# Performance work log

Measured on AMD Instinct MI355X. Metric: run time of the kernel, lower is better.

The kernel has to match this reference:

```python
import jax, jax.numpy as jnp
import numpy as np

NX, NY, T, TP, D, C = 1024, 1024, 512, 512, 128, 8


def _make_dtw_path(t_len, p_len, rng):
    """Random monotone warping path matrix from (0,0) to (t_len-1,p_len-1), as in init_DTW_matrix."""
    M = np.zeros((t_len, p_len), dtype=np.float32)
    k, l = 0, 0
    M[0, 0] = 1.0
    while (k < t_len - 1) or (l < p_len - 1):
        if k == t_len - 1:
            l += 1
        elif l == p_len - 1:
            k += 1
        else:
            m = rng.integers(3)
            if m == 0:
                k += 1
            elif m == 1:
                l += 1
            else:
                k += 1
                l += 1
        M[k, l] = 1.0
    return M


def setup_inputs() -> dict:
    key = jax.random.key(0)
    kx, ky, kc = jax.random.split(key, 3)
    X = jax.random.normal(kx, (NX, T, D), dtype=jnp.float32)
    Y = jax.random.normal(ky, (NY, TP, D), dtype=jnp.float32)
    classe = jax.random.randint(kc, (NX,), 0, C, dtype=jnp.int32)
    rng = np.random.default_rng(0)
    pi = jnp.asarray(np.stack([_make_dtw_path(T, TP, rng) for _ in range(C)]))  # [C, T, TP]
    return {"X": X, "Y": Y, "pi": pi, "classe": classe}


def reference(X, Y, pi, classe):
    """Fused OT-DTW l2 cost matrix: mat_cost[i,j] = sum_{t,tp,d} pi[cl(i)][t,tp]*(X[i,t,d]-Y[j,tp,d])^2.
    Equivalent to OTDTW.mat_cost_OT with metric='l2' (multi-dim branch), vectorized over classes."""
    pi_i = pi[classe]                              # [NX, T, TP] per-sample path matrix
    row = pi_i.sum(-1)                             # [NX, T]  row sums of path
    col = pi.sum(1)                                # [C, TP]  column sums per class
    C1 = jnp.einsum('itd,it->i', X * X, row)       # [NX]
    C2 = jnp.einsum('jpd,cp->cj', Y * Y, col)      # [C, NY]
    XP = jnp.einsum('itd,itp->ipd', X, pi_i)       # [NX, TP, D]
    C3 = jnp.einsum('ipd,jpd->ij', XP, Y)          # [NX, NY]
    return C1[:, None] + C2[classe] - 2.0 * C3
```

## Files before the change

kernel.cpp:

```cpp
#include <hip/hip_runtime.h>
#include <hip/hip_bf16.h>
#include <stdint.h>

namespace {

constexpr int kNX = 1024, kNY = 1024, kT = 512, kTP = 512, kD = 128, kC = 8;
constexpr int kK = kTP * kD;
constexpr int SPLITK = 16;
constexpr int KCH = kK / SPLITK;
constexpr int BKT = 64;
constexpr int NT = KCH / BKT;

typedef short bf16x8 __attribute__((ext_vector_type(8)));
typedef float f32x4 __attribute__((ext_vector_type(4)));

constexpr size_t OFF_YB  = 0;
constexpr size_t OFF_XP  = OFF_YB + (size_t)kNY * kK * 2;
constexpr size_t OFF_YS  = OFF_XP + (size_t)kNX * kK * 2;
constexpr size_t OFF_TS  = OFF_YS + (size_t)kNY * kTP * 4;
constexpr size_t OFF_TE  = OFF_TS + (size_t)kC * kTP * 4;
constexpr size_t OFF_C1  = OFF_TE + (size_t)kC * kTP * 4;
constexpr size_t OFF_C2  = OFF_C1 + (size_t)kNX * 4;

__device__ __forceinline__ void gload16(const __hip_bfloat16* g, __hip_bfloat16* l) {
    __builtin_amdgcn_global_load_lds(
        (const __attribute__((address_space(1))) unsigned int*)g,
        (__attribute__((address_space(3))) unsigned int*)l, 16, 0, 0);
}

__device__ __forceinline__ unsigned short bf(float x) {
    union { __hip_bfloat16 h; unsigned short u; } cv;
    cv.h = __float2bfloat16(x);
    return cv.u;
}

__global__ void init_ranges(int* __restrict__ ts, int* __restrict__ te,
                            float* __restrict__ C1) {
    const int idx = blockIdx.x * 256 + threadIdx.x;
    if (idx < kC * kTP) { ts[idx] = 0x7fffffff; te[idx] = -1; }
    if (idx < kNX) C1[idx] = 0.f;
}

__global__ void pi_scan(const float* __restrict__ pi, int* __restrict__ ts,
                        int* __restrict__ te) {
    const int c = blockIdx.y;
    const int tbase = blockIdx.x * 64;
    const int p = threadIdx.x;
    const float* pic = pi + (size_t)c * kT * kTP;
    int tmin = 0x7fffffff, tmax = -1;
    for (int tt = 0; tt < 64; ++tt) {
        const int t = tbase + tt;
        float v = pic[(size_t)t * kTP + p];
        if (v != 0.f) { if (t < tmin) tmin = t; tmax = t; }
    }
    if (tmax >= 0) {
        atomicMin(&ts[c * kTP + p], tmin);
        atomicMax(&te[c * kTP + p], tmax);
    }
}

__global__ void y_prep(const float* __restrict__ Y, __hip_bfloat16* __restrict__ YB,
                       float* __restrict__ YS) {
    const int j = blockIdx.x;
    const int tid = threadIdx.x;
    const int sub = tid & 31, g = tid >> 5;
    const float4* Yj = (const float4*)(Y + (size_t)j * kTP * kD);
    unsigned short* YBj = (unsigned short*)YB + (size_t)j * kTP * kD;
    for (int p = g; p < kTP; p += 8) {
        float4 y = Yj[p * 32 + sub];
        ushort4 o;
        o.x = bf(y.x); o.y = bf(y.y); o.z = bf(y.z); o.w = bf(y.w);
        *(ushort4*)(YBj + p * kD + sub * 4) = o;
        float s = y.x * y.x + y.y * y.y + y.z * y.z + y.w * y.w;
        #pragma unroll
        for (int o2 = 16; o2; o2 >>= 1) s += __shfl_down(s, o2, 32);
        if (sub == 0) YS[(size_t)j * kTP + p] = s;
    }
}

__global__ void c2_kernel(const float* __restrict__ YS, const int* __restrict__ ts,
                          const int* __restrict__ te, float* __restrict__ C2) {
    const int j = blockIdx.x;
    const int lane = threadIdx.x;
    const float* ys = YS + (size_t)j * kTP;
    for (int c = 0; c < kC; ++c) {
        float s = 0.f;
        for (int p = lane; p < kTP; p += 64) {
            float colv = (float)(te[c * kTP + p] - ts[c * kTP + p] + 1);
            s += ys[p] * colv;
        }
        #pragma unroll
        for (int o = 32; o; o >>= 1) s += __shfl_down(s, o);
        if (lane == 0) C2[c * kNY + j] = s;
    }
}

__global__ __launch_bounds__(256) void xp_kernel(const float* __restrict__ X,
                                                 const int* __restrict__ classe,
                                                 const int* __restrict__ ts,
                                                 const int* __restrict__ te,
                                                 float* __restrict__ C1,
                                                 __hip_bfloat16* __restrict__ XPB) {
    const int i = blockIdx.y, pc = blockIdx.x;
    const int tid = threadIdx.x;
    const int sub = tid & 31, g = tid >> 5;
    const int c = classe[i];
    const float4* Xi = (const float4*)(X + (size_t)i * kT * kD);
    unsigned short* XPi = (unsigned short*)XPB + (size_t)i * kTP * kD;
    float sq = 0.f;
    #pragma unroll
    for (int q = 0; q < 8; ++q) {
        const int p = pc * 64 + q * 8 + g;
        const int t0 = ts[c * kTP + p], t1 = te[c * kTP + p];
        float ax = 0.f, ay = 0.f, az = 0.f, aw = 0.f;
        for (int t = t0; t <= t1; ++t) {
            float4 v = Xi[t * 32 + sub];
            ax += v.x; ay += v.y; az += v.z; aw += v.w;
            sq += v.x * v.x + v.y * v.y + v.z * v.z + v.w * v.w;
        }
        ushort4 o;
        o.x = bf(ax); o.y = bf(ay); o.z = bf(az); o.w = bf(aw);
        *(ushort4*)(XPi + p * kD + sub * 4) = o;
    }
    #pragma unroll
    for (int o = 32; o; o >>= 1) sq += __shfl_down(sq, o);
    __shared__ float red[4];
    if ((tid & 63) == 0) red[tid >> 6] = sq;
    __syncthreads();
    if (tid == 0) atomicAdd(&C1[i], red[0] + red[1] + red[2] + red[3]);
}

__global__ void init_out(const float* __restrict__ C1, const float* __restrict__ C2,
                         const int* __restrict__ classe, float* __restrict__ out) {
    const int i = blockIdx.x;
    const float c1 = C1[i];
    const float* c2 = C2 + (size_t)classe[i] * kNY;
    float* o = out + (size_t)i * kNY;
    for (int j = threadIdx.x; j < kNY; j += 256) o[j] = c1 + c2[j];
}

__global__ __launch_bounds__(512, 2) void gemm_c3(const __hip_bfloat16* __restrict__ A,
                                                  const __hip_bfloat16* __restrict__ B,
                                                  float* __restrict__ out) {
    __shared__ __align__(16) char lds[131072];
    __hip_bfloat16* ldsE = (__hip_bfloat16*)lds;

    const int tid = threadIdx.x;
    const int lane = tid & 63, wv = tid >> 6;
    const int wr = wv >> 2, wc = wv & 3;

    const int bid = blockIdx.x;
    const int swz = (bid & 7) * 32 + (bid >> 3);
    const int z = swz >> 4, t16 = swz & 15;
    const int rowBase = (t16 >> 2) * 256;
    const int colBase = (t16 & 3) * 256;
    const size_t k0base = (size_t)z * KCH;

    const int scol = ((tid & 7) * 8) ^ (((tid >> 3) & 7) * 8);
    const __hip_bfloat16* aSrc[4];
    const __hip_bfloat16* bSrc[4];
    int dstE[4];
    #pragma unroll
    for (int q = 0; q < 4; ++q) {
        const int R = q * 64 + (tid >> 3);
        aSrc[q] = A + (size_t)(rowBase + R) * kK + k0base + scol;
        bSrc[q] = B + (size_t)(colBase + R) * kK + k0base + scol;
        dstE[q] = (q * 512 + tid) * 8;
    }

    const int swzR = (lane & 7) << 4;
    const int aLin = (wr * 128 + (lane & 15)) * 128 + ((lane >> 4) << 4);
    const int bLin = (wc * 64 + (lane & 15)) * 128 + ((lane >> 4) << 4);
    const int aB0 = (aLin) ^ swzR, aB1 = (aLin + 64) ^ swzR;
    const int bB0 = (bLin) ^ swzR, bB1 = (bLin + 64) ^ swzR;

    f32x4 acc[8][4] = {};

    #pragma unroll
    for (int q = 0; q < 4; ++q) gload16(aSrc[q], ldsE + dstE[q]);
    #pragma unroll
    for (int q = 0; q < 4; ++q) gload16(bSrc[q], ldsE + 16384 + dstE[q]);

    int buf = 0;
    for (int t = 0; t < NT; ++t) {
        asm volatile("s_waitcnt vmcnt(0)" ::: "memory");
        __builtin_amdgcn_s_barrier();
        asm volatile("" ::: "memory");

        const int koff = (t + 1) * BKT;
        const int bufB = buf * 65536;
        const int nBufE = (buf ^ 1) * 32768;

        if (t + 1 < NT) {
            #pragma unroll
            for (int q = 0; q < 4; ++q) gload16(aSrc[q] + koff, ldsE + nBufE + dstE[q]);
        }

        #pragma unroll
        for (int qd = 0; qd < 4; ++qd) {
            const int mh = qd & 1, nh = qd >> 1;
            bf16x8 af[4][2], bfr[2][2];
            #pragma unroll
            for (int m = 0; m < 4; ++m) {
                af[m][0] = *(const bf16x8*)(lds + bufB + aB0 + mh * 8192 + m * 2048);
                af[m][1] = *(const bf16x8*)(lds + bufB + aB1 + mh * 8192 + m * 2048);
            }
            #pragma unroll
            for (int n = 0; n < 2; ++n) {
                bfr[n][0] = *(const bf16x8*)(lds + bufB + 32768 + bB0 + nh * 4096 + n * 2048);
                bfr[n][1] = *(const bf16x8*)(lds + bufB + 32768 + bB1 + nh * 4096 + n * 2048);
            }
            __builtin_amdgcn_s_setprio(1);
            #pragma unroll
            for (int m = 0; m < 4; ++m)
                #pragma unroll
                for (int n = 0; n < 2; ++n) {
                    acc[mh * 4 + m][nh * 2 + n] = __builtin_amdgcn_mfma_f32_16x16x32_bf16(
                        af[m][0], bfr[n][0], acc[mh * 4 + m][nh * 2 + n], 0, 0, 0);
                    acc[mh * 4 + m][nh * 2 + n] = __builtin_amdgcn_mfma_f32_16x16x32_bf16(
                        af[m][1], bfr[n][1], acc[mh * 4 + m][nh * 2 + n], 0, 0, 0);
                }
            __builtin_amdgcn_s_setprio(0);

            if (qd == 0 && t + 1 < NT) {
                #pragma unroll
                for (int q = 0; q < 4; ++q)
                    gload16(bSrc[q] + koff, ldsE + nBufE + 16384 + dstE[q]);
            }
        }
        buf ^= 1;
    }

    #pragma unroll
    for (int mi = 0; mi < 8; ++mi) {
        #pragma unroll
        for (int ni = 0; ni < 4; ++ni) {
            #pragma unroll
            for (int jj = 0; jj < 4; ++jj) {
                const int R = rowBase + wr * 128 + mi * 16 + (lane >> 4) * 4 + jj;
                const int Cc = colBase + wc * 64 + ni * 16 + (lane & 15);
                atomicAdd(&out[(size_t)R * kNY + Cc], -2.0f * acc[mi][ni][jj]);
            }
        }
    }
}

}

extern "C" void kernel_launch(void* const* d_in, const int* in_sizes, int n_in,
                              void* d_out, int out_size, void* d_ws, size_t ws_size,
                              hipStream_t stream) {
    const float* X = (const float*)d_in[0];
    const float* Y = (const float*)d_in[1];
    const float* pi = (const float*)d_in[2];
    const int* classe = (const int*)d_in[3];
    float* out = (float*)d_out;

    char* ws = (char*)d_ws;
    __hip_bfloat16* YB = (__hip_bfloat16*)(ws + OFF_YB);
    __hip_bfloat16* XPB = (__hip_bfloat16*)(ws + OFF_XP);
    float* YS = (float*)(ws + OFF_YS);
    int* ts = (int*)(ws + OFF_TS);
    int* te = (int*)(ws + OFF_TE);
    float* C1 = (float*)(ws + OFF_C1);
    float* C2 = (float*)(ws + OFF_C2);

    init_ranges<<<(kC * kTP + 255) / 256, 256, 0, stream>>>(ts, te, C1);
    pi_scan<<<dim3(kT / 64, kC), kTP, 0, stream>>>(pi, ts, te);
    y_prep<<<kNY, 256, 0, stream>>>(Y, YB, YS);
    c2_kernel<<<kNY, 64, 0, stream>>>(YS, ts, te, C2);
    xp_kernel<<<dim3(8, kNX), 256, 0, stream>>>(X, classe, ts, te, C1, XPB);
    init_out<<<kNX, 256, 0, stream>>>(C1, C2, classe, out);
    gemm_c3<<<(kNX / 256) * (kNY / 256) * SPLITK, 512, 0, stream>>>(XPB, YB, out);
}
```

Before: 387.6 us.

## Merge Y prep, C2 reduction and XP build into one kernel; fold bias into GEMM

Combines y_prep, c2_kernel and xp_kernel into a single prep_main launch that splits block indices between Y conversion (now computing the C2 per-class sums directly from LDS-cached path counts) and XP accumulation. It drops the YS intermediate buffer. The split-K slice z==0 of the GEMM adds C1+C2 while doing its atomic adds, and a memset replaces init_out. This cuts launches and an extra pass over the output, but adds a per-element bias gather in the GEMM epilogue and a 16KB LDS fill per Y block.

```diff
diff --git a/kernel.cpp b/kernel.cpp
--- a/kernel.cpp
+++ b/kernel.cpp
@@ -16,8 +16,7 @@
 
 constexpr size_t OFF_YB  = 0;
 constexpr size_t OFF_XP  = OFF_YB + (size_t)kNY * kK * 2;
-constexpr size_t OFF_YS  = OFF_XP + (size_t)kNX * kK * 2;
-constexpr size_t OFF_TS  = OFF_YS + (size_t)kNY * kTP * 4;
+constexpr size_t OFF_TS  = OFF_XP + (size_t)kNX * kK * 2;
 constexpr size_t OFF_TE  = OFF_TS + (size_t)kC * kTP * 4;
 constexpr size_t OFF_C1  = OFF_TE + (size_t)kC * kTP * 4;
 constexpr size_t OFF_C2  = OFF_C1 + (size_t)kNX * 4;
@@ -59,88 +58,90 @@
     }
 }
 
-__global__ void y_prep(const float* __restrict__ Y, __hip_bfloat16* __restrict__ YB,
-                       float* __restrict__ YS) {
-    const int j = blockIdx.x;
-    const int tid = threadIdx.x;
-    const int sub = tid & 31, g = tid >> 5;
-    const float4* Yj = (const float4*)(Y + (size_t)j * kTP * kD);
-    unsigned short* YBj = (unsigned short*)YB + (size_t)j * kTP * kD;
-    for (int p = g; p < kTP; p += 8) {
-        float4 y = Yj[p * 32 + sub];
-        ushort4 o;
-        o.x = bf(y.x); o.y = bf(y.y); o.z = bf(y.z); o.w = bf(y.w);
-        *(ushort4*)(YBj + p * kD + sub * 4) = o;
-        float s = y.x * y.x + y.y * y.y + y.z * y.z + y.w * y.w;
-        #pragma unroll
-        for (int o2 = 16; o2; o2 >>= 1) s += __shfl_down(s, o2, 32);
-        if (sub == 0) YS[(size_t)j * kTP + p] = s;
-    }
-}
-
-__global__ void c2_kernel(const float* __restrict__ YS, const int* __restrict__ ts,
-                          const int* __restrict__ te, float* __restrict__ C2) {
-    const int j = blockIdx.x;
-    const int lane = threadIdx.x;
-    const float* ys = YS + (size_t)j * kTP;
-    for (int c = 0; c < kC; ++c) {
-        float s = 0.f;
-        for (int p = lane; p < kTP; p += 64) {
-            float colv = (float)(te[c * kTP + p] - ts[c * kTP + p] + 1);
-            s += ys[p] * colv;
-        }
-        #pragma unroll
-        for (int o = 32; o; o >>= 1) s += __shfl_down(s, o);
-        if (lane == 0) C2[c * kNY + j] = s;
-    }
-}
-
-__global__ __launch_bounds__(256) void xp_kernel(const float* __restrict__ X,
+__global__ __launch_bounds__(256) void prep_main(const float* __restrict__ Y,
+                                                 const float* __restrict__ X,
                                                  const int* __restrict__ classe,
                                                  const int* __restrict__ ts,
                                                  const int* __restrict__ te,
+                                                 __hip_bfloat16* __restrict__ YB,
+                                                 __hip_bfloat16* __restrict__ XPB,
                                                  float* __restrict__ C1,
-                                                 __hip_bfloat16* __restrict__ XPB) {
-    const int i = blockIdx.y, pc = blockIdx.x;
+                                                 float* __restrict__ C2) {
+    const int bid = blockIdx.x;
     const int tid = threadIdx.x;
     const int sub = tid & 31, g = tid >> 5;
-    const int c = classe[i];
-    const float4* Xi = (const float4*)(X + (size_t)i * kT * kD);
-    unsigned short* XPi = (unsigned short*)XPB + (size_t)i * kTP * kD;
-    float sq = 0.f;
-    #pragma unroll
-    for (int q = 0; q < 8; ++q) {
-        const int p = pc * 64 + q * 8 + g;
-        const int t0 = ts[c * kTP + p], t1 = te[c * kTP + p];
-        float ax = 0.f, ay = 0.f, az = 0.f, aw = 0.f;
-        for (int t = t0; t <= t1; ++t) {
-            float4 v = Xi[t * 32 + sub];
-            ax += v.x; ay += v.y; az += v.z; aw += v.w;
-            sq += v.x * v.x + v.y * v.y + v.z * v.z + v.w * v.w;
-        }
-        ushort4 o;
-        o.x = bf(ax); o.y = bf(ay); o.z = bf(az); o.w = bf(aw);
-        *(ushort4*)(XPi + p * kD + sub * 4) = o;
-    }
-    #pragma unroll
-    for (int o = 32; o; o >>= 1) sq += __shfl_down(sq, o);
-    __shared__ float red[4];
-    if ((tid & 63) == 0) red[tid >> 6] = sq;
-    __syncthreads();
-    if (tid == 0) atomicAdd(&C1[i], red[0] + red[1] + red[2] + red[3]);
-}
-
-__global__ void init_out(const float* __restrict__ C1, const float* __restrict__ C2,
-                         const int* __restrict__ classe, float* __restrict__ out) {
-    const int i = blockIdx.x;
-    const float c1 = C1[i];
-    const float* c2 = C2 + (size_t)classe[i] * kNY;
-    float* o = out + (size_t)i * kNY;
-    for (int j = threadIdx.x; j < kNY; j += 256) o[j] = c1 + c2[j];
+
+    if (bid < kNY) {
+        const int j = bid;
+        __shared__ float cntL[kC * kTP];
+        for (int idx = tid; idx < kC * kTP; idx += 256)
+            cntL[idx] = (float)(te[idx] - ts[idx] + 1);
+        __syncthreads();
+
+        const float4* Yj = (const float4*)(Y + (size_t)j * kTP * kD);
+        unsigned short* YBj = (unsigned short*)YB + (size_t)j * kTP * kD;
+        float c2acc[kC] = {};
+        for (int p = g; p < kTP; p += 8) {
+            float4 y = Yj[p * 32 + sub];
+            ushort4 o;
+            o.x = bf(y.x); o.y = bf(y.y); o.z = bf(y.z); o.w = bf(y.w);
+            *(ushort4*)(YBj + p * kD + sub * 4) = o;
+            float s = y.x * y.x + y.y * y.y + y.z * y.z + y.w * y.w;
+            #pragma unroll
+            for (int o2 = 16; o2; o2 >>= 1) s += __shfl_xor(s, o2, 32);
+            if (sub == 0) {
+                #pragma unroll
+                for (int c = 0; c < kC; ++c) c2acc[c] += cntL[c * kTP + p] * s;
+            }
+        }
+        __syncthreads();
+        __shared__ float c2red[8][kC];
+        if (sub == 0) {
+            #pragma unroll
+            for (int c = 0; c < kC; ++c) c2red[g][c] = c2acc[c];
+        }
+        __syncthreads();
+        if (tid < kC) {
+            float s = 0.f;
+            #pragma unroll
+            for (int q = 0; q < 8; ++q) s += c2red[q][tid];
+            C2[tid * kNY + j] = s;
+        }
+    } else {
+        const int b2 = bid - kNY;
+        const int i = b2 >> 3, pc = b2 & 7;
+        const int c = classe[i];
+        const float4* Xi = (const float4*)(X + (size_t)i * kT * kD);
+        unsigned short* XPi = (unsigned short*)XPB + (size_t)i * kTP * kD;
+        float sq = 0.f;
+        #pragma unroll
+        for (int q = 0; q < 8; ++q) {
+            const int p = pc * 64 + q * 8 + g;
+            const int t0 = ts[c * kTP + p], t1 = te[c * kTP + p];
+            float ax = 0.f, ay = 0.f, az = 0.f, aw = 0.f;
+            for (int t = t0; t <= t1; ++t) {
+                float4 v = Xi[t * 32 + sub];
+                ax += v.x; ay += v.y; az += v.z; aw += v.w;
+                sq += v.x * v.x + v.y * v.y + v.z * v.z + v.w * v.w;
+            }
+            ushort4 o;
+            o.x = bf(ax); o.y = bf(ay); o.z = bf(az); o.w = bf(aw);
+            *(ushort4*)(XPi + p * kD + sub * 4) = o;
+        }
+        #pragma unroll
+        for (int o = 32; o; o >>= 1) sq += __shfl_down(sq, o);
+        __shared__ float red[4];
+        if ((tid & 63) == 0) red[tid >> 6] = sq;
+        __syncthreads();
+        if (tid == 0) atomicAdd(&C1[i], red[0] + red[1] + red[2] + red[3]);
+    }
 }
 
 __global__ __launch_bounds__(512, 2) void gemm_c3(const __hip_bfloat16* __restrict__ A,
                                                   const __hip_bfloat16* __restrict__ B,
+                                                  const float* __restrict__ C1,
+                                                  const float* __restrict__ C2,
+                                                  const int* __restrict__ classe,
                                                   float* __restrict__ out) {
     __shared__ __align__(16) char lds[131072];
     __hip_bfloat16* ldsE = (__hip_bfloat16*)lds;
@@ -231,6 +232,7 @@
         buf ^= 1;
     }
 
+    const bool addBase = (z == 0);
     #pragma unroll
     for (int mi = 0; mi < 8; ++mi) {
         #pragma unroll
@@ -239,7 +241,9 @@
             for (int jj = 0; jj < 4; ++jj) {
                 const int R = rowBase + wr * 128 + mi * 16 + (lane >> 4) * 4 + jj;
                 const int Cc = colBase + wc * 64 + ni * 16 + (lane & 15);
-                atomicAdd(&out[(size_t)R * kNY + Cc], -2.0f * acc[mi][ni][jj]);
+                float v = -2.0f * acc[mi][ni][jj];
+                if (addBase) v += C1[R] + C2[(size_t)classe[R] * kNY + Cc];
+                atomicAdd(&out[(size_t)R * kNY + Cc], v);
             }
         }
     }
@@ -259,17 +263,14 @@
     char* ws = (char*)d_ws;
     __hip_bfloat16* YB = (__hip_bfloat16*)(ws + OFF_YB);
     __hip_bfloat16* XPB = (__hip_bfloat16*)(ws + OFF_XP);
-    float* YS = (float*)(ws + OFF_YS);
     int* ts = (int*)(ws + OFF_TS);
     int* te = (int*)(ws + OFF_TE);
     float* C1 = (float*)(ws + OFF_C1);
     float* C2 = (float*)(ws + OFF_C2);
 
+    hipMemsetAsync(out, 0, (size_t)out_size * sizeof(float), stream);
     init_ranges<<<(kC * kTP + 255) / 256, 256, 0, stream>>>(ts, te, C1);
     pi_scan<<<dim3(kT / 64, kC), kTP, 0, stream>>>(pi, ts, te);
-    y_prep<<<kNY, 256, 0, stream>>>(Y, YB, YS);
-    c2_kernel<<<kNY, 64, 0, stream>>>(YS, ts, te, C2);
-    xp_kernel<<<dim3(8, kNX), 256, 0, stream>>>(X, classe, ts, te, C1, XPB);
-    init_out<<<kNX, 256, 0, stream>>>(C1, C2, classe, out);
-    gemm_c3<<<(kNX / 256) * (kNY / 256) * SPLITK, 512, 0, stream>>>(XPB, YB, out);
-}
+    prep_main<<<kNY + kNX * 8, 256, 0, stream>>>(Y, X, classe, ts, te, YB, XPB, C1, C2);
+    gemm_c3<<<(kNX / 256) * (kNY / 256) * SPLITK, 512, 0, stream>>>(XPB, YB, C1, C2, classe, out);
+}
```

Result: slower. 413.0 us (+6.6%).
